# Performance work log

Hardware: AMD Instinct MI355X
Metric: run time of the kernel (lower is better)

The kernel has to match this reference:

```python
import jax, jax.numpy as jnp
import numpy as np

E = 524288
B = 16
NODE_IN = 128
EDGE_IN = 64
GLOBAL_IN = 64
HIDDEN = 256
EDGE_OUT = 64
CAT_IN = EDGE_IN + 2 * NODE_IN + GLOBAL_IN  # 384


def setup_inputs() -> dict:
    key = jax.random.key(0)
    ks = jax.random.split(key, 9)
    src = jax.random.normal(ks[0], (E, NODE_IN), dtype=jnp.float32)
    dest = jax.random.normal(ks[1], (E, NODE_IN), dtype=jnp.float32)
    edge_attr = jax.random.normal(ks[2], (E, EDGE_IN), dtype=jnp.float32)
    u = jax.random.normal(ks[3], (B, GLOBAL_IN), dtype=jnp.float32)
    batch = jnp.sort(jax.random.randint(ks[4], (E,), 0, B, dtype=jnp.int64))
    # MLP params (torch Linear default init scale ~1/sqrt(fan_in))
    W1 = jax.random.normal(ks[5], (CAT_IN, HIDDEN), dtype=jnp.float32) / np.sqrt(CAT_IN)
    b1 = jax.random.normal(ks[6], (HIDDEN,), dtype=jnp.float32) / np.sqrt(CAT_IN)
    W2 = jax.random.normal(ks[7], (HIDDEN, EDGE_OUT), dtype=jnp.float32) / np.sqrt(HIDDEN)
    b2 = jax.random.normal(ks[8], (EDGE_OUT,), dtype=jnp.float32) / np.sqrt(HIDDEN)
    return {"src": src, "dest": dest, "edge_attr": edge_attr, "u": u,
            "batch": batch, "W1": W1, "b1": b1, "W2": W2, "b2": b2}


def reference(src, dest, edge_attr, u, batch, W1, b1, W2, b2):
    # gather global features per edge, concat, 2-layer MLP with ReLU
    x = jnp.concatenate([src, dest, edge_attr, u[batch]], axis=1)  # [E, 384]
    h = jax.nn.relu(x @ W1 + b1)                                   # [E, hidden]
    return h @ W2 + b2                                             # [E, edge_out]
```

## Files before the change

kernel.cpp:

```cpp
#include <hip/hip_runtime.h>

typedef __bf16 bf16_t;
typedef bf16_t bf16x8 __attribute__((ext_vector_type(8)));
typedef float f32x4 __attribute__((ext_vector_type(4)));
typedef unsigned short u16;
typedef unsigned int u32;

#define E_TOT 524288
#define MT 64
#define NBLK (E_TOT / MT)

__device__ __forceinline__ u16 f2bf(float f) {
  u32 u = __builtin_bit_cast(u32, f);
  u += 0x7FFFu + ((u >> 16) & 1u);
  return (u16)(u >> 16);
}

__device__ __forceinline__ bf16x8 pack8(f32x4 a, f32x4 b) {
  bf16x8 p;
  p[0] = (bf16_t)a[0]; p[1] = (bf16_t)a[1]; p[2] = (bf16_t)a[2]; p[3] = (bf16_t)a[3];
  p[4] = (bf16_t)b[0]; p[5] = (bf16_t)b[1]; p[6] = (bf16_t)b[2]; p[7] = (bf16_t)b[3];
  return p;
}

__device__ __forceinline__ void gload_lds16(const void* g, void* l) {
  __builtin_amdgcn_global_load_lds(
      (const __attribute__((address_space(1))) u32*)g,
      (__attribute__((address_space(3))) u32*)l, 16, 0, 0);
}

__global__ void prep_w1ts(const float* __restrict__ W1, u16* __restrict__ W1Ts) {
  int t = blockIdx.x * 256 + threadIdx.x;
  if (t < 384 * 256) {
    int U = t >> 3, e = t & 7;
    int kb = U >> 11, rem = U & 2047;
    int n = rem >> 3, jswz = rem & 7;
    int k = kb * 64 + ((jswz ^ (n & 7)) << 3) + e;
    W1Ts[t] = f2bf(W1[k * 256 + n]);
  }
}

__global__ void prep_w2ts(const float* __restrict__ W2, u16* __restrict__ W2Ts) {
  int t = blockIdx.x * 256 + threadIdx.x;
  if (t < 64 * 256) {
    int U = t >> 3, e = t & 7;
    int n = U >> 5, uj = U & 31;
    int k = ((uj ^ (n & 7)) << 3) + e;
    W2Ts[t] = f2bf(W2[k * 64 + n]);
  }
}

__global__ void __launch_bounds__(256, 2) edge_fused(
    const float* __restrict__ src, const float* __restrict__ dst,
    const float* __restrict__ ea, const float* __restrict__ u,
    const int* __restrict__ batch, const u16* __restrict__ Wall,
    const float* __restrict__ b1, const float* __restrict__ b2,
    float* __restrict__ out)
{
  __shared__ __align__(16) u16 smem[36864];
  u16* As  = smem;
  u16* Wb0 = smem + 4096;
  u16* Wb1 = smem + 20480;
  u16* W2s = Wb0;
  u16* Hs  = Wb1;

  const int t    = threadIdx.x;
  const int wid  = t >> 6;
  const int lane = t & 63;
  const int lr   = lane & 15;
  const int lg   = lane >> 4;
  const int e0   = blockIdx.x * MT;
  const int r    = t >> 2;
  const int cg   = (t & 3) << 4;
  const int j0   = (t & 3) * 2;

  f32x4 av[6][4];
  #pragma unroll
  for (int c = 0; c < 6; ++c) {
    const float* rowp;
    if (c < 2)       rowp = src + (size_t)(e0 + r) * 128 + c * 64;
    else if (c < 4)  rowp = dst + (size_t)(e0 + r) * 128 + (c - 2) * 64;
    else if (c == 4) rowp = ea + (size_t)(e0 + r) * 64;
    else             rowp = u + (size_t)batch[e0 + r] * 64;
    av[c][0] = *(const f32x4*)(rowp + cg + 0);
    av[c][1] = *(const f32x4*)(rowp + cg + 4);
    av[c][2] = *(const f32x4*)(rowp + cg + 8);
    av[c][3] = *(const f32x4*)(rowp + cg + 12);
  }

  #pragma unroll
  for (int it = 0; it < 8; ++it) {
    int ubase = (it * 4 + wid) * 64;
    gload_lds16(Wall + ((size_t)ubase + lane) * 8, &Wb0[ubase * 8]);
  }

  bf16x8 ar[6][2];
  #pragma unroll
  for (int c = 0; c < 6; ++c) {
    ar[c][0] = pack8(av[c][0], av[c][1]);
    ar[c][1] = pack8(av[c][2], av[c][3]);
  }

  f32x4 acc[4][4];
  #pragma unroll
  for (int i = 0; i < 4; ++i)
    #pragma unroll
    for (int j = 0; j < 4; ++j)
      acc[i][j] = (f32x4){0.f, 0.f, 0.f, 0.f};

  #pragma unroll
  for (int kb = 0; kb < 6; ++kb) {
    u16* Wc = (kb & 1) ? Wb1 : Wb0;
    u16* Wn = (kb & 1) ? Wb0 : Wb1;

    *(bf16x8*)&As[r * 64 + ((j0 ^ (r & 7)) << 3)]       = ar[kb][0];
    *(bf16x8*)&As[r * 64 + (((j0 + 1) ^ (r & 7)) << 3)] = ar[kb][1];

    #pragma unroll
    for (int it = 0; it < 8; ++it) {
      int ubase = (it * 4 + wid) * 64;
      gload_lds16(Wall + ((size_t)(kb + 1) * 2048 + ubase + lane) * 8, &Wn[ubase * 8]);
    }

    asm volatile("s_waitcnt vmcnt(8)\n\ts_waitcnt lgkmcnt(0)" ::: "memory");
    __builtin_amdgcn_sched_barrier(0);
    __builtin_amdgcn_s_barrier();

    __builtin_amdgcn_s_setprio(1);
    #pragma unroll
    for (int ks = 0; ks < 2; ++ks) {
      bf16x8 af[4];
      #pragma unroll
      for (int mf = 0; mf < 4; ++mf) {
        int row = mf * 16 + lr;
        af[mf] = *(const bf16x8*)&As[row * 64 + (((ks * 4 + lg) ^ (row & 7)) << 3)];
      }
      #pragma unroll
      for (int nf = 0; nf < 4; ++nf) {
        int n = wid * 64 + nf * 16 + lr;
        bf16x8 bfr = *(const bf16x8*)&Wc[n * 64 + (((ks * 4 + lg) ^ (n & 7)) << 3)];
        #pragma unroll
        for (int mf = 0; mf < 4; ++mf)
          acc[mf][nf] = __builtin_amdgcn_mfma_f32_16x16x32_bf16(af[mf], bfr, acc[mf][nf], 0, 0, 0);
      }
    }
    __builtin_amdgcn_s_setprio(0);
    __builtin_amdgcn_s_barrier();
  }

  asm volatile("s_waitcnt vmcnt(0)" ::: "memory");

  float bias1[4];
  #pragma unroll
  for (int nf = 0; nf < 4; ++nf) bias1[nf] = b1[wid * 64 + nf * 16 + lr];
  #pragma unroll
  for (int mf = 0; mf < 4; ++mf)
    #pragma unroll
    for (int nf = 0; nf < 4; ++nf)
      #pragma unroll
      for (int rr = 0; rr < 4; ++rr) {
        int row = mf * 16 + lg * 4 + rr;
        int col = wid * 64 + nf * 16 + lr;
        float v = fmaxf(acc[mf][nf][rr] + bias1[nf], 0.f);
        *(bf16_t*)&Hs[row * 256 + ((((col >> 3) ^ (row & 7)) << 3) | (col & 7))] = (bf16_t)v;
      }
  __syncthreads();

  f32x4 acc2[4];
  #pragma unroll
  for (int nf = 0; nf < 4; ++nf) acc2[nf] = (f32x4){0.f, 0.f, 0.f, 0.f};
  const int rowA = wid * 16 + lr;
  #pragma unroll
  for (int ks = 0; ks < 8; ++ks) {
    bf16x8 a = *(const bf16x8*)&Hs[rowA * 256 + (((ks * 4 + lg) ^ (rowA & 7)) << 3)];
    #pragma unroll
    for (int nf = 0; nf < 4; ++nf) {
      int n = nf * 16 + lr;
      bf16x8 b = *(const bf16x8*)&W2s[n * 256 + (((ks * 4 + lg) ^ (n & 7)) << 3)];
      acc2[nf] = __builtin_amdgcn_mfma_f32_16x16x32_bf16(a, b, acc2[nf], 0, 0, 0);
    }
  }

  #pragma unroll
  for (int nf = 0; nf < 4; ++nf) {
    float bb = b2[nf * 16 + lr];
    #pragma unroll
    for (int rr = 0; rr < 4; ++rr) {
      int row = e0 + wid * 16 + lg * 4 + rr;
      out[(size_t)row * 64 + nf * 16 + lr] = acc2[nf][rr] + bb;
    }
  }
}

extern "C" void kernel_launch(void* const* d_in, const int* in_sizes, int n_in,
                              void* d_out, int out_size, void* d_ws, size_t ws_size,
                              hipStream_t stream) {
  const float* src  = (const float*)d_in[0];
  const float* dst  = (const float*)d_in[1];
  const float* ea   = (const float*)d_in[2];
  const float* u    = (const float*)d_in[3];
  const int* batch  = (const int*)d_in[4];
  const float* W1   = (const float*)d_in[5];
  const float* b1   = (const float*)d_in[6];
  const float* W2   = (const float*)d_in[7];
  const float* b2   = (const float*)d_in[8];
  float* out = (float*)d_out;

  u16* W1Ts = (u16*)d_ws;
  u16* W2Ts = W1Ts + 384 * 256;

  prep_w1ts<<<(384 * 256 + 255) / 256, 256, 0, stream>>>(W1, W1Ts);
  prep_w2ts<<<(64 * 256 + 255) / 256, 256, 0, stream>>>(W2, W2Ts);
  edge_fused<<<NBLK, 256, 0, stream>>>(src, dst, ea, u, batch, W1Ts, b1, b2, out);
}
```

Measured before the change: 236.9 us.

## Double edge tile per block with 8 waves and stream activation loads per K chunk

Raises the edge tile from 64 to 128 rows and the block from 256 to 512 threads, so each W1 chunk staged in LDS is shared by twice as many rows. Activation loads move from an up-front load of all six chunks to a two-deep register pipeline that issues chunk kb+2 after the barrier, which lowers register pressure. The second GEMM runs in two halves over the 64-row H buffer with extra barriers. In exchange, the looser launch bounds and larger LDS may reduce occupancy, and the split epilogue adds synchronization.

```diff
diff --git a/kernel.cpp b/kernel.cpp
--- a/kernel.cpp
+++ b/kernel.cpp
@@ -7,7 +7,7 @@
 typedef unsigned int u32;
 
 #define E_TOT 524288
-#define MT 64
+#define MT 128
 #define NBLK (E_TOT / MT)
 
 __device__ __forceinline__ u16 f2bf(float f) {
@@ -50,17 +50,17 @@
   }
 }
 
-__global__ void __launch_bounds__(256, 2) edge_fused(
+__global__ void __launch_bounds__(512) edge_fused(
     const float* __restrict__ src, const float* __restrict__ dst,
     const float* __restrict__ ea, const float* __restrict__ u,
     const int* __restrict__ batch, const u16* __restrict__ Wall,
     const float* __restrict__ b1, const float* __restrict__ b2,
     float* __restrict__ out)
 {
-  __shared__ __align__(16) u16 smem[36864];
+  __shared__ __align__(16) u16 smem[40960];
   u16* As  = smem;
-  u16* Wb0 = smem + 4096;
-  u16* Wb1 = smem + 20480;
+  u16* Wb0 = smem + 8192;
+  u16* Wb1 = smem + 24576;
   u16* W2s = Wb0;
   u16* Hs  = Wb1;
 
@@ -69,37 +69,36 @@
   const int lane = t & 63;
   const int lr   = lane & 15;
   const int lg   = lane >> 4;
+  const int wr   = wid >> 2;
+  const int wc   = wid & 3;
   const int e0   = blockIdx.x * MT;
   const int r    = t >> 2;
   const int cg   = (t & 3) << 4;
   const int j0   = (t & 3) * 2;
 
-  f32x4 av[6][4];
-  #pragma unroll
-  for (int c = 0; c < 6; ++c) {
+  auto issueA = [&](int c, f32x4* av) {
     const float* rowp;
     if (c < 2)       rowp = src + (size_t)(e0 + r) * 128 + c * 64;
     else if (c < 4)  rowp = dst + (size_t)(e0 + r) * 128 + (c - 2) * 64;
     else if (c == 4) rowp = ea + (size_t)(e0 + r) * 64;
     else             rowp = u + (size_t)batch[e0 + r] * 64;
-    av[c][0] = *(const f32x4*)(rowp + cg + 0);
-    av[c][1] = *(const f32x4*)(rowp + cg + 4);
-    av[c][2] = *(const f32x4*)(rowp + cg + 8);
-    av[c][3] = *(const f32x4*)(rowp + cg + 12);
-  }
-
-  #pragma unroll
-  for (int it = 0; it < 8; ++it) {
-    int ubase = (it * 4 + wid) * 64;
-    gload_lds16(Wall + ((size_t)ubase + lane) * 8, &Wb0[ubase * 8]);
-  }
-
-  bf16x8 ar[6][2];
-  #pragma unroll
-  for (int c = 0; c < 6; ++c) {
-    ar[c][0] = pack8(av[c][0], av[c][1]);
-    ar[c][1] = pack8(av[c][2], av[c][3]);
-  }
+    av[0] = *(const f32x4*)(rowp + cg + 0);
+    av[1] = *(const f32x4*)(rowp + cg + 4);
+    av[2] = *(const f32x4*)(rowp + cg + 8);
+    av[3] = *(const f32x4*)(rowp + cg + 12);
+  };
+  auto stageW = [&](int chunk, u16* Wn) {
+    #pragma unroll
+    for (int it = 0; it < 4; ++it) {
+      int ubase = (it * 8 + wid) * 64;
+      gload_lds16(Wall + ((size_t)chunk * 2048 + ubase + lane) * 8, &Wn[ubase * 8]);
+    }
+  };
+
+  f32x4 avA[4], avB[4];
+  issueA(0, avA);
+  issueA(1, avB);
+  stageW(0, Wb0);
 
   f32x4 acc[4][4];
   #pragma unroll
@@ -112,19 +111,22 @@
   for (int kb = 0; kb < 6; ++kb) {
     u16* Wc = (kb & 1) ? Wb1 : Wb0;
     u16* Wn = (kb & 1) ? Wb0 : Wb1;
-
-    *(bf16x8*)&As[r * 64 + ((j0 ^ (r & 7)) << 3)]       = ar[kb][0];
-    *(bf16x8*)&As[r * 64 + (((j0 + 1) ^ (r & 7)) << 3)] = ar[kb][1];
-
-    #pragma unroll
-    for (int it = 0; it < 8; ++it) {
-      int ubase = (it * 4 + wid) * 64;
-      gload_lds16(Wall + ((size_t)(kb + 1) * 2048 + ubase + lane) * 8, &Wn[ubase * 8]);
-    }
-
-    asm volatile("s_waitcnt vmcnt(8)\n\ts_waitcnt lgkmcnt(0)" ::: "memory");
+    f32x4* av = (kb & 1) ? avB : avA;
+
+    {
+      bf16x8 lo = pack8(av[0], av[1]);
+      bf16x8 hi = pack8(av[2], av[3]);
+      *(bf16x8*)&As[r * 64 + ((j0 ^ (r & 7)) << 3)]       = lo;
+      *(bf16x8*)&As[r * 64 + (((j0 + 1) ^ (r & 7)) << 3)] = hi;
+    }
+    stageW(kb + 1, Wn);
+
+    if (kb < 5) asm volatile("s_waitcnt vmcnt(8) lgkmcnt(0)" ::: "memory");
+    else        asm volatile("s_waitcnt vmcnt(4) lgkmcnt(0)" ::: "memory");
     __builtin_amdgcn_sched_barrier(0);
     __builtin_amdgcn_s_barrier();
+
+    if (kb < 4) issueA(kb + 2, av);
 
     __builtin_amdgcn_s_setprio(1);
     #pragma unroll
@@ -132,12 +134,12 @@
       bf16x8 af[4];
       #pragma unroll
       for (int mf = 0; mf < 4; ++mf) {
-        int row = mf * 16 + lr;
+        int row = wr * 64 + mf * 16 + lr;
         af[mf] = *(const bf16x8*)&As[row * 64 + (((ks * 4 + lg) ^ (row & 7)) << 3)];
       }
       #pragma unroll
       for (int nf = 0; nf < 4; ++nf) {
-        int n = wid * 64 + nf * 16 + lr;
+        int n = wc * 64 + nf * 16 + lr;
         bf16x8 bfr = *(const bf16x8*)&Wc[n * 64 + (((ks * 4 + lg) ^ (n & 7)) << 3)];
         #pragma unroll
         for (int mf = 0; mf < 4; ++mf)
@@ -152,43 +154,52 @@
 
   float bias1[4];
   #pragma unroll
-  for (int nf = 0; nf < 4; ++nf) bias1[nf] = b1[wid * 64 + nf * 16 + lr];
-  #pragma unroll
-  for (int mf = 0; mf < 4; ++mf)
-    #pragma unroll
-    for (int nf = 0; nf < 4; ++nf)
+  for (int nf = 0; nf < 4; ++nf) bias1[nf] = b1[wc * 64 + nf * 16 + lr];
+
+  const int mf2  = wid >> 1;
+  const int nf2a = (wid & 1) * 2;
+  const int nf2b = nf2a + 1;
+  const float bb_a = b2[nf2a * 16 + lr];
+  const float bb_b = b2[nf2b * 16 + lr];
+  const int rowA = mf2 * 16 + lr;
+
+  #pragma unroll
+  for (int half = 0; half < 2; ++half) {
+    if (wr == half) {
       #pragma unroll
-      for (int rr = 0; rr < 4; ++rr) {
-        int row = mf * 16 + lg * 4 + rr;
-        int col = wid * 64 + nf * 16 + lr;
-        float v = fmaxf(acc[mf][nf][rr] + bias1[nf], 0.f);
-        *(bf16_t*)&Hs[row * 256 + ((((col >> 3) ^ (row & 7)) << 3) | (col & 7))] = (bf16_t)v;
-      }
-  __syncthreads();
-
-  f32x4 acc2[4];
-  #pragma unroll
-  for (int nf = 0; nf < 4; ++nf) acc2[nf] = (f32x4){0.f, 0.f, 0.f, 0.f};
-  const int rowA = wid * 16 + lr;
-  #pragma unroll
-  for (int ks = 0; ks < 8; ++ks) {
-    bf16x8 a = *(const bf16x8*)&Hs[rowA * 256 + (((ks * 4 + lg) ^ (rowA & 7)) << 3)];
-    #pragma unroll
-    for (int nf = 0; nf < 4; ++nf) {
-      int n = nf * 16 + lr;
-      bf16x8 b = *(const bf16x8*)&W2s[n * 256 + (((ks * 4 + lg) ^ (n & 7)) << 3)];
-      acc2[nf] = __builtin_amdgcn_mfma_f32_16x16x32_bf16(a, b, acc2[nf], 0, 0, 0);
-    }
-  }
-
-  #pragma unroll
-  for (int nf = 0; nf < 4; ++nf) {
-    float bb = b2[nf * 16 + lr];
+      for (int mf = 0; mf < 4; ++mf)
+        #pragma unroll
+        for (int nf = 0; nf < 4; ++nf)
+          #pragma unroll
+          for (int rr = 0; rr < 4; ++rr) {
+            int row = mf * 16 + lg * 4 + rr;
+            int col = wc * 64 + nf * 16 + lr;
+            float v = fmaxf(acc[mf][nf][rr] + bias1[nf], 0.f);
+            *(bf16_t*)&Hs[row * 256 + ((((col >> 3) ^ (row & 7)) << 3) | (col & 7))] = (bf16_t)v;
+          }
+    }
+    __syncthreads();
+
+    f32x4 acc2a = (f32x4){0.f, 0.f, 0.f, 0.f};
+    f32x4 acc2b = (f32x4){0.f, 0.f, 0.f, 0.f};
+    #pragma unroll
+    for (int ks = 0; ks < 8; ++ks) {
+      bf16x8 a = *(const bf16x8*)&Hs[rowA * 256 + (((ks * 4 + lg) ^ (rowA & 7)) << 3)];
+      int nA = nf2a * 16 + lr;
+      int nB = nf2b * 16 + lr;
+      bf16x8 ba = *(const bf16x8*)&W2s[nA * 256 + (((ks * 4 + lg) ^ (nA & 7)) << 3)];
+      bf16x8 bb = *(const bf16x8*)&W2s[nB * 256 + (((ks * 4 + lg) ^ (nB & 7)) << 3)];
+      acc2a = __builtin_amdgcn_mfma_f32_16x16x32_bf16(a, ba, acc2a, 0, 0, 0);
+      acc2b = __builtin_amdgcn_mfma_f32_16x16x32_bf16(a, bb, acc2b, 0, 0, 0);
+    }
+
     #pragma unroll
     for (int rr = 0; rr < 4; ++rr) {
-      int row = e0 + wid * 16 + lg * 4 + rr;
-      out[(size_t)row * 64 + nf * 16 + lr] = acc2[nf][rr] + bb;
-    }
+      int row = e0 + half * 64 + mf2 * 16 + lg * 4 + rr;
+      out[(size_t)row * 64 + nf2a * 16 + lr] = acc2a[rr] + bb_a;
+      out[(size_t)row * 64 + nf2b * 16 + lr] = acc2b[rr] + bb_b;
+    }
+    __syncthreads();
   }
 }
 
@@ -211,5 +222,5 @@
 
   prep_w1ts<<<(384 * 256 + 255) / 256, 256, 0, stream>>>(W1, W1Ts);
   prep_w2ts<<<(64 * 256 + 255) / 256, 256, 0, stream>>>(W2, W2Ts);
-  edge_fused<<<NBLK, 256, 0, stream>>>(src, dst, ea, u, batch, W1Ts, b1, b2, out);
-}
+  edge_fused<<<NBLK, 512, 0, stream>>>(src, dst, ea, u, batch, W1Ts, b1, b2, out);
+}
```

New measurement: 257.5 us. 1.09x slower.
